# Optimization experiments

Measured on AMD Instinct MI355X. Metric: run time of the kernel, lower is better.

## Reference

```python
import jax, jax.numpy as jnp
import numpy as np

B, C, Hd, Wd = 8, 256, 64, 64
NUM_HEAD = 4
RATIO = 0.25
OUT_CH = int(NUM_HEAD * C * RATIO)      # 256
HEAD_DIM = OUT_CH // NUM_HEAD           # 64
EPS = 1e-5


def conv1x1(x, w, b=None):
    # x: [B,Ci,H,W], w: [Co,Ci]
    y = jnp.einsum('bchw,oc->bohw', x, w)
    if b is not None:
        y = y + b[None, :, None, None]
    return y


def setup_inputs() -> dict:
    key = jax.random.key(0)
    ks = jax.random.split(key, 16)
    s = lambda fan: 1.0 / np.sqrt(fan)
    return {
        'key':   jax.random.normal(ks[0], (B, C, Hd, Wd), jnp.float32),
        'query': jax.random.normal(ks[1], (B, C, Hd, Wd), jnp.float32),
        'wq': jax.random.normal(ks[2], (OUT_CH, C), jnp.float32) * s(C),
        'bq': jax.random.normal(ks[3], (OUT_CH,), jnp.float32) * 0.01,
        'wk': jax.random.normal(ks[4], (OUT_CH, C), jnp.float32) * s(C),
        'bk': jax.random.normal(ks[5], (OUT_CH,), jnp.float32) * 0.01,
        'wv': jax.random.normal(ks[6], (OUT_CH, C), jnp.float32) * s(C),
        'bv': jax.random.normal(ks[7], (OUT_CH,), jnp.float32) * 0.01,
        'wW': jax.random.normal(ks[8], (C, HEAD_DIM), jnp.float32) * s(HEAD_DIM),
        'bn_gamma': jnp.ones((C,), jnp.float32),
        'bn_beta': jnp.zeros((C,), jnp.float32),
        'bn_mean': jax.random.normal(ks[9], (C,), jnp.float32) * 0.1,
        'bn_var': jax.random.uniform(ks[10], (C,), jnp.float32, 0.5, 1.5),
        'w3': jax.random.normal(ks[11], (C, 2 * C, 3, 3), jnp.float32) * s(2 * C * 9),
        'b3': jax.random.normal(ks[12], (C,), jnp.float32) * 0.01,
        'w1': jax.random.normal(ks[13], (C, C), jnp.float32) * s(C),
        'b1': jax.random.normal(ks[14], (C,), jnp.float32) * 0.01,
    }


def reference(key, query, wq, bq, wk, bk, wv, bv, wW,
              bn_gamma, bn_beta, bn_mean, bn_var, w3, b3, w1, b1):
    b, c, h, w = query.shape
    q = conv1x1(query, wq, bq).reshape(b, NUM_HEAD, HEAD_DIM, h, w)
    k = conv1x1(key, wk, bk).reshape(b, NUM_HEAD, HEAD_DIM, h, w)
    v = conv1x1(key, wv, bv).reshape(b, NUM_HEAD, HEAD_DIM, h, w)

    att = (q * k).sum(axis=2) / np.sqrt(OUT_CH)          # [b, num_head, h, w]
    sm = jax.nn.softmax(att, axis=1)[:, :, None]         # softmax over heads
    weighted = (v * sm).sum(axis=1)                      # [b, head_dim, h, w]

    # W: 1x1 conv (no bias) + BatchNorm (inference)
    out = conv1x1(weighted, wW)
    inv = bn_gamma / jnp.sqrt(bn_var + EPS)
    out = out * inv[None, :, None, None] + (bn_beta - bn_mean * inv)[None, :, None, None]

    # fuse: ConvBlock (reflect-pad 3x3 conv + ELU) then 1x1 conv
    x = jnp.concatenate([key, out], axis=1)              # [b, 2C, h, w]
    x = jnp.pad(x, ((0, 0), (0, 0), (1, 1), (1, 1)), mode='reflect')
    x = jax.lax.conv_general_dilated(x, w3, (1, 1), 'VALID',
                                     dimension_numbers=('NCHW', 'OIHW', 'NCHW'))
    x = jax.nn.elu(x + b3[None, :, None, None])
    return conv1x1(x, w1, b1)
```

## Files before the change

kernel.cpp:

```cpp
#include <hip/hip_runtime.h>
#include <hip/hip_bf16.h>

typedef unsigned short u16;
typedef unsigned int u32;
typedef short bf16x8 __attribute__((ext_vector_type(8)));
typedef float f32x4 __attribute__((ext_vector_type(4)));

#define NPX 32768

__device__ __forceinline__ u16 f2bf(float f) {
  union { float f; u32 u; } v; v.f = f;
  return (u16)((v.u + 0x7FFFu + ((v.u >> 16) & 1u)) >> 16);
}

__device__ __forceinline__ void gload16(const u16* g, u16* l) {
  __builtin_amdgcn_global_load_lds(
      (const __attribute__((address_space(1))) void*)g,
      (__attribute__((address_space(3))) void*)l, 16, 0, 0);
}


__global__ __launch_bounds__(256) void prep_small(
    const float* __restrict__ wq, const float* __restrict__ wk,
    const float* __restrict__ wv, const float* __restrict__ w1,
    const float* __restrict__ wW, const float* __restrict__ gamma,
    const float* __restrict__ beta, const float* __restrict__ mean,
    const float* __restrict__ var,
    u16* __restrict__ wqb, u16* __restrict__ wkb, u16* __restrict__ wvb,
    u16* __restrict__ w1b, u16* __restrict__ wWpb, float* __restrict__ bWp) {
  int idx = blockIdx.x * 256 + threadIdx.x;
  if (idx < 65536) {
    int o = idx >> 8, c = idx & 255;
    int dst = (c >> 5) * 8192 + o * 32 + ((c >> 3) & 3) * 8 + (c & 7);
    wqb[dst] = f2bf(wq[idx]);
    wkb[dst] = f2bf(wk[idx]);
    wvb[dst] = f2bf(wv[idx]);
    w1b[dst] = f2bf(w1[idx]);
  } else if (idx < 65536 + 16384) {
    int j = idx - 65536;
    int o = j >> 6, c = j & 63;
    float inv = gamma[o] * rsqrtf(var[o] + 1e-5f);
    int dst = (c >> 5) * 8192 + o * 32 + ((c >> 3) & 3) * 8 + (c & 7);
    wWpb[dst] = f2bf(wW[j] * inv);
  } else if (idx < 65536 + 16384 + 256) {
    int o = idx - 65536 - 16384;
    float inv = gamma[o] * rsqrtf(var[o] + 1e-5f);
    bWp[o] = beta[o] - mean[o] * inv;
  }
}

__global__ __launch_bounds__(256) void prep_w3t(const float* __restrict__ w3,
                                                u16* __restrict__ w3c) {
  int idx = blockIdx.x * 256 + threadIdx.x;
  int o = idx >> 9, c = idx & 511;
  int cb = c >> 5;
  int lk = (c >> 3) & 3, e = c & 7;
  #pragma unroll
  for (int t = 0; t < 9; ++t)
    w3c[(size_t)(cb * 9 + t) * 8192 + o * 32 + lk * 8 + e] =
        f2bf(w3[idx * 9 + t]);
}

__global__ __launch_bounds__(256, 2) void attn_kernel(
    const float* __restrict__ qsrc, const float* __restrict__ ksrc,
    u16* __restrict__ xcat,
    const u16* __restrict__ wqb, const u16* __restrict__ wkb, const u16* __restrict__ wvb,
    const float* __restrict__ bq, const float* __restrict__ bk, const float* __restrict__ bv,
    const u16* __restrict__ wWpb, const float* __restrict__ bWp) {
  __shared__ __align__(16) char smem[74752];
  u16* aq = (u16*)smem;
  u16* ak = (u16*)(smem + 32768);
  u16* tile = (u16*)(smem + 65536);
  float* att_s = (float*)(smem + 65536);
  u16* wsum = (u16*)(smem + 66560);
  float* wbuf = (float*)smem;
  u16* ob = (u16*)smem;

  int tid = threadIdx.x;
  int lane = tid & 63, wv_ = tid >> 6;
  int lc = lane & 15, lk = lane >> 4;
  int px0 = blockIdx.x * 64;
  int b = px0 >> 12, hw0 = px0 & 4095;

  #pragma unroll
  for (int t = 0; t < 8; ++t) {
    const float* src = (t < 4) ? qsrc : ksrc;
    int cc = t & 3;
    #pragma unroll
    for (int i = 0; i < 4; ++i) {
      int idx = tid + 256 * i;
      int c = idx >> 4, p4 = idx & 15;
      const float4 v = *(const float4*)&src[(size_t)(b * 256 + cc * 64 + c) * 4096 + hw0 + p4 * 4];
      u32 lo = f2bf(v.x) | ((u32)f2bf(v.y) << 16);
      u32 hi = f2bf(v.z) | ((u32)f2bf(v.w) << 16);
      *(uint2*)&tile[c * 72 + p4 * 4] = make_uint2(lo, hi);
    }
    __syncthreads();
    int px = tid >> 2, cq = tid & 3;
    u32 vv[8];
    #pragma unroll
    for (int i = 0; i < 8; ++i) {
      u16 a = tile[(cq * 16 + 2 * i) * 72 + px];
      u16 bb = tile[(cq * 16 + 2 * i + 1) * 72 + px];
      vv[i] = a | ((u32)bb << 16);
    }
    u16* dstl = (t < 4) ? aq : ak;
    int c8 = cc * 8 + cq * 2;
    *(uint4*)(dstl + px * 256 + (c8 ^ (px & 7)) * 8) = make_uint4(vv[0], vv[1], vv[2], vv[3]);
    *(uint4*)(dstl + px * 256 + ((c8 + 1) ^ (px & 7)) * 8) = make_uint4(vv[4], vv[5], vv[6], vv[7]);
    if (t >= 4) {
      u16* dp = xcat + (size_t)(px0 + px) * 512 + cc * 64 + cq * 16;
      *(uint4*)dp = make_uint4(vv[0], vv[1], vv[2], vv[3]);
      *(uint4*)(dp + 8) = make_uint4(vv[4], vv[5], vv[6], vv[7]);
    }
    __syncthreads();
  }

  f32x4 zero4 = {0.f, 0.f, 0.f, 0.f};
  f32x4 accq[4][4], acck[4][4];
  #pragma unroll
  for (int mi = 0; mi < 4; ++mi)
    #pragma unroll
    for (int nj = 0; nj < 4; ++nj) { accq[mi][nj] = zero4; acck[mi][nj] = zero4; }

  #pragma unroll
  for (int kk = 0; kk < 8; ++kk) {
    bf16x8 afq[4], afk[4], bfq[4], bfk[4];
    #pragma unroll
    for (int mi = 0; mi < 4; ++mi) {
      int px = mi * 16 + lc;
      int s = (kk * 4 + lk) ^ (px & 7);
      afq[mi] = *(const bf16x8*)(aq + px * 256 + s * 8);
      afk[mi] = *(const bf16x8*)(ak + px * 256 + s * 8);
    }
    #pragma unroll
    for (int nj = 0; nj < 4; ++nj) {
      int n = wv_ * 64 + nj * 16 + lc;
      bfq[nj] = *(const bf16x8*)(wqb + kk * 8192 + n * 32 + lk * 8);
      bfk[nj] = *(const bf16x8*)(wkb + kk * 8192 + n * 32 + lk * 8);
    }
    #pragma unroll
    for (int mi = 0; mi < 4; ++mi)
      #pragma unroll
      for (int nj = 0; nj < 4; ++nj) {
        accq[mi][nj] = __builtin_amdgcn_mfma_f32_16x16x32_bf16(afq[mi], bfq[nj], accq[mi][nj], 0, 0, 0);
        acck[mi][nj] = __builtin_amdgcn_mfma_f32_16x16x32_bf16(afk[mi], bfk[nj], acck[mi][nj], 0, 0, 0);
      }
  }

  #pragma unroll
  for (int nj = 0; nj < 4; ++nj) {
    float bqv = bq[wv_ * 64 + nj * 16 + lc];
    float bkv = bk[wv_ * 64 + nj * 16 + lc];
    #pragma unroll
    for (int mi = 0; mi < 4; ++mi)
      #pragma unroll
      for (int j = 0; j < 4; ++j) { accq[mi][nj][j] += bqv; acck[mi][nj][j] += bkv; }
  }

  float smx[4][4];
  #pragma unroll
  for (int mi = 0; mi < 4; ++mi)
    #pragma unroll
    for (int j = 0; j < 4; ++j) {
      float p = 0.f;
      #pragma unroll
      for (int nj = 0; nj < 4; ++nj) p += accq[mi][nj][j] * acck[mi][nj][j];
      p += __shfl_xor(p, 1);
      p += __shfl_xor(p, 2);
      p += __shfl_xor(p, 4);
      p += __shfl_xor(p, 8);
      float a = p * 0.0625f;
      smx[mi][j] = a;
      if (lc == 0) att_s[wv_ * 64 + mi * 16 + lk * 4 + j] = a;
    }
  __syncthreads();
  #pragma unroll
  for (int mi = 0; mi < 4; ++mi)
    #pragma unroll
    for (int j = 0; j < 4; ++j) {
      int px = mi * 16 + lk * 4 + j;
      float a0 = att_s[px], a1 = att_s[64 + px], a2 = att_s[128 + px], a3 = att_s[192 + px];
      float mx = fmaxf(fmaxf(a0, a1), fmaxf(a2, a3));
      float e0 = __expf(a0 - mx), e1 = __expf(a1 - mx);
      float e2 = __expf(a2 - mx), e3 = __expf(a3 - mx);
      float den = e0 + e1 + e2 + e3;
      float ew = wv_ == 0 ? e0 : (wv_ == 1 ? e1 : (wv_ == 2 ? e2 : e3));
      smx[mi][j] = ew / den;
    }

  f32x4 accv[4][4];
  #pragma unroll
  for (int mi = 0; mi < 4; ++mi)
    #pragma unroll
    for (int nj = 0; nj < 4; ++nj) accv[mi][nj] = zero4;
  #pragma unroll
  for (int kk = 0; kk < 8; ++kk) {
    bf16x8 af[4], bfr[4];
    #pragma unroll
    for (int mi = 0; mi < 4; ++mi) {
      int px = mi * 16 + lc;
      int s = (kk * 4 + lk) ^ (px & 7);
      af[mi] = *(const bf16x8*)(ak + px * 256 + s * 8);
    }
    #pragma unroll
    for (int nj = 0; nj < 4; ++nj) {
      int n = wv_ * 64 + nj * 16 + lc;
      bfr[nj] = *(const bf16x8*)(wvb + kk * 8192 + n * 32 + lk * 8);
    }
    #pragma unroll
    for (int mi = 0; mi < 4; ++mi)
      #pragma unroll
      for (int nj = 0; nj < 4; ++nj)
        accv[mi][nj] = __builtin_amdgcn_mfma_f32_16x16x32_bf16(af[mi], bfr[nj], accv[mi][nj], 0, 0, 0);
  }
  #pragma unroll
  for (int nj = 0; nj < 4; ++nj) {
    float bvv = bv[wv_ * 64 + nj * 16 + lc];
    #pragma unroll
    for (int mi = 0; mi < 4; ++mi)
      #pragma unroll
      for (int j = 0; j < 4; ++j) accv[mi][nj][j] += bvv;
  }
  __syncthreads();

  #pragma unroll
  for (int mi = 0; mi < 4; ++mi)
    #pragma unroll
    for (int nj = 0; nj < 4; ++nj)
      #pragma unroll
      for (int j = 0; j < 4; ++j) {
        int px = mi * 16 + lk * 4 + j;
        wbuf[(wv_ * 64 + px) * 64 + nj * 16 + lc] = smx[mi][j] * accv[mi][nj][j];
      }
  __syncthreads();

  #pragma unroll
  for (int i = 0; i < 2; ++i) {
    int idx = tid + 256 * i;
    int px = idx >> 3, c = idx & 7;
    float a8[8] = {0.f, 0.f, 0.f, 0.f, 0.f, 0.f, 0.f, 0.f};
    #pragma unroll
    for (int h = 0; h < 4; ++h) {
      const float4* p = (const float4*)(wbuf + ((h * 64 + px) * 64 + c * 8));
      float4 u0 = p[0], u1 = p[1];
      a8[0] += u0.x; a8[1] += u0.y; a8[2] += u0.z; a8[3] += u0.w;
      a8[4] += u1.x; a8[5] += u1.y; a8[6] += u1.z; a8[7] += u1.w;
    }
    u32 p0 = f2bf(a8[0]) | ((u32)f2bf(a8[1]) << 16);
    u32 p1 = f2bf(a8[2]) | ((u32)f2bf(a8[3]) << 16);
    u32 p2 = f2bf(a8[4]) | ((u32)f2bf(a8[5]) << 16);
    u32 p3 = f2bf(a8[6]) | ((u32)f2bf(a8[7]) << 16);
    *(uint4*)(wsum + px * 64 + (c ^ (px & 7)) * 8) = make_uint4(p0, p1, p2, p3);
  }
  __syncthreads();

  f32x4 a4[4][4];
  #pragma unroll
  for (int mi = 0; mi < 4; ++mi)
    #pragma unroll
    for (int nj = 0; nj < 4; ++nj) a4[mi][nj] = zero4;
  #pragma unroll
  for (int kk = 0; kk < 2; ++kk) {
    bf16x8 af[4], bfr[4];
    #pragma unroll
    for (int mi = 0; mi < 4; ++mi) {
      int px = mi * 16 + lc;
      int s = (kk * 4 + lk) ^ (px & 7);
      af[mi] = *(const bf16x8*)(wsum + px * 64 + s * 8);
    }
    #pragma unroll
    for (int nj = 0; nj < 4; ++nj) {
      int n = wv_ * 64 + nj * 16 + lc;
      bfr[nj] = *(const bf16x8*)(wWpb + kk * 8192 + n * 32 + lk * 8);
    }
    #pragma unroll
    for (int mi = 0; mi < 4; ++mi)
      #pragma unroll
      for (int nj = 0; nj < 4; ++nj)
        a4[mi][nj] = __builtin_amdgcn_mfma_f32_16x16x32_bf16(af[mi], bfr[nj], a4[mi][nj], 0, 0, 0);
  }
  #pragma unroll
  for (int nj = 0; nj < 4; ++nj) {
    int o = wv_ * 64 + nj * 16 + lc;
    float bb = bWp[o];
    #pragma unroll
    for (int mi = 0; mi < 4; ++mi)
      #pragma unroll
      for (int j = 0; j < 4; ++j) {
        int px = mi * 16 + lk * 4 + j;
        ob[px * 264 + o] = f2bf(a4[mi][nj][j] + bb);
      }
  }
  __syncthreads();
  #pragma unroll
  for (int i = 0; i < 8; ++i) {
    int idx = tid + 256 * i;
    int px = idx >> 5, c8 = idx & 31;
    *(uint4*)(xcat + (size_t)(px0 + px) * 512 + 256 + c8 * 8) =
        *(const uint4*)(ob + px * 264 + c8 * 8);
  }
}

__global__ __launch_bounds__(512, 2) void conv3_kernel(
    const u16* __restrict__ xcat, const u16* __restrict__ w3c,
    const float* __restrict__ b3, const u16* __restrict__ w1b,
    const float* __restrict__ b1, float* __restrict__ out) {
  extern __shared__ __align__(16) u16 smem[];
  u16* xb0 = smem;
  u16* xb1 = smem + 8704;
  u16* wbase = smem + 17408;

  int tid = threadIdx.x;
  int lane = tid & 63, wave = tid >> 6;
  int lc = lane & 15, lk = lane >> 4;
  int wr = wave >> 2, wc = wave & 3;
  int sbid = (blockIdx.x & 7) * 32 + (blockIdx.x >> 3);
  int b = sbid >> 5, r0 = (sbid & 31) * 2;

  int gx0, gx1, gx2;
  #pragma unroll
  for (int i = 0; i < 3; ++i) {
    int c = (i == 0) ? tid : (i == 1 ? tid + 512 : 1024 + lane);
    int row = c / 272, rem = c - row * 272;
    int s = rem / 68, px = rem - s * 68;
    px = px < 66 ? px : 65;
    int h_in = r0 - 1 + row; h_in = h_in < 0 ? 1 : (h_in > 63 ? 62 : h_in);
    int w_in = px - 1;       w_in = w_in < 0 ? 1 : (w_in > 63 ? 62 : w_in);
    int g = ((b * 64 + h_in) * 64 + w_in) * 512 + s * 8;
    if (i == 0) gx0 = g; else if (i == 1) gx1 = g; else gx2 = g;
  }
  int gw0 = (tid ^ ((tid >> 3) & 7)) * 8;
  int p1_ = tid + 512;
  int gw1 = (p1_ ^ ((p1_ >> 3) & 7)) * 8;

#define STAGE_W(dst, slab)                                                      \
  do {                                                                          \
    const u16* ws_ = w3c + (size_t)(slab) * 8192;                               \
    gload16(ws_ + gw0, (dst) + (size_t)tid * 8);                                \
    gload16(ws_ + gw1, (dst) + (size_t)(tid + 512) * 8);                        \
  } while (0)

#define STAGE_X(dst, cb_)                                                       \
  do {                                                                          \
    gload16(xcat + gx0 + (cb_) * 32, (dst) + (size_t)tid * 8);                  \
    gload16(xcat + gx1 + (cb_) * 32, (dst) + (size_t)(tid + 512) * 8);          \
    if (wave == 0) gload16(xcat + gx2 + (cb_) * 32, (dst) + (size_t)(1024 + lane) * 8); \
  } while (0)

  f32x4 zero4 = {0.f, 0.f, 0.f, 0.f};
  f32x4 acc[4][4];
  #pragma unroll
  for (int mi = 0; mi < 4; ++mi)
    #pragma unroll
    for (int nj = 0; nj < 4; ++nj) acc[mi][nj] = zero4;

#define COMPUTE(TAP, XB, WIDX)                                                  \
  do {                                                                          \
    const u16* wcur_ = wbase + (size_t)(WIDX) * 8192;                           \
    bf16x8 af[4], bfr[4];                                                       \
    _Pragma("unroll") for (int mi = 0; mi < 4; ++mi)                            \
      af[mi] = *(const bf16x8*)((XB) +                                          \
          (size_t)(((wr + (TAP) / 3) * 4 + lk) * 68 + mi * 16 + lc + (TAP) % 3) * 8); \
    _Pragma("unroll") for (int nj = 0; nj < 4; ++nj) {                          \
      int j_ = (wc * 64 + nj * 16 + lc) * 4 + lk;                               \
      bfr[nj] = *(const bf16x8*)(wcur_ + (size_t)(j_ ^ ((j_ >> 3) & 7)) * 8);   \
    }                                                                           \
    __builtin_amdgcn_s_setprio(1);                                              \
    _Pragma("unroll") for (int mi = 0; mi < 4; ++mi)                            \
      _Pragma("unroll") for (int nj = 0; nj < 4; ++nj)                          \
        acc[mi][nj] = __builtin_amdgcn_mfma_f32_16x16x32_bf16(                  \
            af[mi], bfr[nj], acc[mi][nj], 0, 0, 0);                             \
    __builtin_amdgcn_s_setprio(0);                                              \
  } while (0)

  STAGE_W(wbase, 0);
  STAGE_W(wbase + 8192, 1);
  STAGE_X(xb0, 0);
  asm volatile("s_waitcnt vmcnt(0)\n\ts_barrier" ::: "memory");

  for (int cb = 0; cb < 15; ++cb) {
    const u16* xcur = (cb & 1) ? xb1 : xb0;
    u16* xnxt = (cb & 1) ? xb0 : xb1;
    int c4 = cb & 3;
    int base = cb * 9;
#define PH(TAP)                                                                 \
    STAGE_W(wbase + (size_t)((c4 + (TAP) + 2) & 3) * 8192, base + (TAP) + 2);   \
    if ((TAP) == 4) STAGE_X(xnxt, cb + 1);                                      \
    if ((TAP) < 4) {                                                            \
      asm volatile("s_waitcnt vmcnt(4)\n\ts_barrier" ::: "memory");             \
    } else if (wave == 0) {                                                     \
      asm volatile("s_waitcnt vmcnt(7)\n\ts_barrier" ::: "memory");             \
    } else {                                                                    \
      asm volatile("s_waitcnt vmcnt(6)\n\ts_barrier" ::: "memory");             \
    }                                                                           \
    COMPUTE(TAP, xcur, (c4 + (TAP)) & 3);
    PH(0) PH(1) PH(2) PH(3) PH(4) PH(5) PH(6) PH(7) PH(8)
#undef PH
  }
  {
    const u16* xcur = xb1;
#define PH15(TAP, WN)                                                           \
    if ((TAP) < 7) STAGE_W(wbase + (size_t)((3 + (TAP) + 2) & 3) * 8192, 137 + (TAP)); \
    asm volatile("s_waitcnt vmcnt(" #WN ")\n\ts_barrier" ::: "memory");         \
    COMPUTE(TAP, xcur, (3 + (TAP)) & 3);
    PH15(0, 4) PH15(1, 4) PH15(2, 4) PH15(3, 4) PH15(4, 4) PH15(5, 4) PH15(6, 4)
    PH15(7, 2) PH15(8, 0)
#undef PH15
  }
#undef STAGE_W
#undef STAGE_X
#undef COMPUTE

  __syncthreads();

  u16* eb = smem;
  #pragma unroll
  for (int nj = 0; nj < 4; ++nj) {
    int o = wc * 64 + nj * 16 + lc;
    float bias = b3[o];
    #pragma unroll
    for (int mi = 0; mi < 4; ++mi)
      #pragma unroll
      for (int j = 0; j < 4; ++j) {
        int p = wr * 64 + mi * 16 + lk * 4 + j;
        float v = acc[mi][nj][j] + bias;
        v = v > 0.f ? v : (__expf(v) - 1.f);
        eb[p * 260 + o] = f2bf(v);
      }
  }
  __syncthreads();

  f32x4 acc2[4][4];
  #pragma unroll
  for (int mi = 0; mi < 4; ++mi)
    #pragma unroll
    for (int nj = 0; nj < 4; ++nj) acc2[mi][nj] = zero4;
  #pragma unroll
  for (int kk = 0; kk < 8; ++kk) {
    bf16x8 af[4], bfr[4];
    #pragma unroll
    for (int mi = 0; mi < 4; ++mi)
      af[mi] = *(const bf16x8*)(eb + (size_t)(wr * 64 + mi * 16 + lc) * 260 + kk * 32 + lk * 8);
    #pragma unroll
    for (int nj = 0; nj < 4; ++nj)
      bfr[nj] = *(const bf16x8*)(w1b + kk * 8192 + (wc * 64 + nj * 16 + lc) * 32 + lk * 8);
    #pragma unroll
    for (int mi = 0; mi < 4; ++mi)
      #pragma unroll
      for (int nj = 0; nj < 4; ++nj)
        acc2[mi][nj] = __builtin_amdgcn_mfma_f32_16x16x32_bf16(af[mi], bfr[nj], acc2[mi][nj], 0, 0, 0);
  }
  #pragma unroll
  for (int nj = 0; nj < 4; ++nj) {
    int o = wc * 64 + nj * 16 + lc;
    float bias = b1[o];
    #pragma unroll
    for (int mi = 0; mi < 4; ++mi) {
      float4 v;
      v.x = acc2[mi][nj][0] + bias;
      v.y = acc2[mi][nj][1] + bias;
      v.z = acc2[mi][nj][2] + bias;
      v.w = acc2[mi][nj][3] + bias;
      *(float4*)&out[(size_t)(b * 256 + o) * 4096 + (r0 + wr) * 64 + mi * 16 + lk * 4] = v;
    }
  }
}

extern "C" void kernel_launch(void* const* d_in, const int* in_sizes, int n_in,
                              void* d_out, int out_size, void* d_ws, size_t ws_size,
                              hipStream_t stream) {
  const float* key   = (const float*)d_in[0];
  const float* query = (const float*)d_in[1];
  const float* wq    = (const float*)d_in[2];
  const float* bq    = (const float*)d_in[3];
  const float* wk    = (const float*)d_in[4];
  const float* bk    = (const float*)d_in[5];
  const float* wv    = (const float*)d_in[6];
  const float* bv    = (const float*)d_in[7];
  const float* wW    = (const float*)d_in[8];
  const float* gamma = (const float*)d_in[9];
  const float* beta  = (const float*)d_in[10];
  const float* mean  = (const float*)d_in[11];
  const float* var   = (const float*)d_in[12];
  const float* w3    = (const float*)d_in[13];
  const float* b3    = (const float*)d_in[14];
  const float* w1    = (const float*)d_in[15];
  const float* b1    = (const float*)d_in[16];
  float* out = (float*)d_out;

  char* ws = (char*)d_ws;
  u16* xcat  = (u16*)(ws + 16777216);
  u16* w3t   = (u16*)(ws + 67108864);
  u16* wqb   = (u16*)(ws + 69468160);
  u16* wkb   = (u16*)(ws + 69599232);
  u16* wvb   = (u16*)(ws + 69730304);
  u16* w1b   = (u16*)(ws + 69861376);
  u16* wWpb  = (u16*)(ws + 69992448);
  float* bWp = (float*)(ws + 70025216);

  (void)hipFuncSetAttribute((const void*)conv3_kernel,
                            hipFuncAttributeMaxDynamicSharedMemorySize, 100352);

  prep_small<<<321, 256, 0, stream>>>(wq, wk, wv, w1, wW, gamma, beta, mean, var,
                                      wqb, wkb, wvb, w1b, wWpb, bWp);
  prep_w3t<<<512, 256, 0, stream>>>(w3, w3t);
  attn_kernel<<<512, 256, 0, stream>>>(query, key, xcat, wqb, wkb, wvb,
                                       bq, bk, bv, wWpb, bWp);
  conv3_kernel<<<256, 512, 100352, stream>>>(xcat, w3t, b3, w1b, b1, out);
}
```

Before: 122.6 us.

## Load conv3 weights straight into registers and drop LDS weight staging

The 3x3 conv kernel no longer stages weight slabs through shared memory. Each wave now reads its B-fragments from global memory into a three-deep register ring, prefetched three taps ahead. The activation tile layout changes to pixel-major with four channel slots, the per-tap barriers are removed so there is only one barrier per channel block, and shared memory shrinks to a static 66 KB array. This cuts LDS traffic and synchronisation, at the cost of more VGPRs, the loss of the 2-blocks-per-CU launch bound, and weight loads that each wave issues redundantly from global/L2.

```diff
diff --git a/kernel.cpp b/kernel.cpp
--- a/kernel.cpp
+++ b/kernel.cpp
@@ -302,14 +302,13 @@
   }
 }
 
-__global__ __launch_bounds__(512, 2) void conv3_kernel(
+__global__ __launch_bounds__(512) void conv3_kernel(
     const u16* __restrict__ xcat, const u16* __restrict__ w3c,
     const float* __restrict__ b3, const u16* __restrict__ w1b,
     const float* __restrict__ b1, float* __restrict__ out) {
-  extern __shared__ __align__(16) u16 smem[];
+  __shared__ __align__(16) u16 smem[33792];
   u16* xb0 = smem;
   u16* xb1 = smem + 8704;
-  u16* wbase = smem + 17408;
 
   int tid = threadIdx.x;
   int lane = tid & 63, wave = tid >> 6;
@@ -322,30 +321,32 @@
   #pragma unroll
   for (int i = 0; i < 3; ++i) {
     int c = (i == 0) ? tid : (i == 1 ? tid + 512 : 1024 + lane);
-    int row = c / 272, rem = c - row * 272;
-    int s = rem / 68, px = rem - s * 68;
+    int q = c >> 2, slot = c & 3;
+    int row = q / 68, px = q - row * 68;
     px = px < 66 ? px : 65;
     int h_in = r0 - 1 + row; h_in = h_in < 0 ? 1 : (h_in > 63 ? 62 : h_in);
     int w_in = px - 1;       w_in = w_in < 0 ? 1 : (w_in > 63 ? 62 : w_in);
-    int g = ((b * 64 + h_in) * 64 + w_in) * 512 + s * 8;
+    int g = ((b * 64 + h_in) * 64 + w_in) * 512 + slot * 8;
     if (i == 0) gx0 = g; else if (i == 1) gx1 = g; else gx2 = g;
   }
-  int gw0 = (tid ^ ((tid >> 3) & 7)) * 8;
-  int p1_ = tid + 512;
-  int gw1 = (p1_ ^ ((p1_ >> 3) & 7)) * 8;
-
-#define STAGE_W(dst, slab)                                                      \
-  do {                                                                          \
-    const u16* ws_ = w3c + (size_t)(slab) * 8192;                               \
-    gload16(ws_ + gw0, (dst) + (size_t)tid * 8);                                \
-    gload16(ws_ + gw1, (dst) + (size_t)(tid + 512) * 8);                        \
-  } while (0)
+  int wo0 = ((wc * 64 + lc) * 4 + lk) * 8;
 
 #define STAGE_X(dst, cb_)                                                       \
   do {                                                                          \
+    asm volatile("" ::: "memory");                                              \
     gload16(xcat + gx0 + (cb_) * 32, (dst) + (size_t)tid * 8);                  \
     gload16(xcat + gx1 + (cb_) * 32, (dst) + (size_t)(tid + 512) * 8);          \
-    if (wave == 0) gload16(xcat + gx2 + (cb_) * 32, (dst) + (size_t)(1024 + lane) * 8); \
+    gload16(xcat + gx2 + (cb_) * 32, (dst) + (size_t)(1024 + lane) * 8);        \
+    asm volatile("" ::: "memory");                                              \
+  } while (0)
+
+#define PREF_W(SLOT, SLAB)                                                      \
+  do {                                                                          \
+    const u16* ws_ = w3c + (size_t)(SLAB) * 8192 + wo0;                         \
+    Wr[SLOT][0] = *(const bf16x8*)(ws_);                                        \
+    Wr[SLOT][1] = *(const bf16x8*)(ws_ + 512);                                  \
+    Wr[SLOT][2] = *(const bf16x8*)(ws_ + 1024);                                 \
+    Wr[SLOT][3] = *(const bf16x8*)(ws_ + 1536);                                 \
   } while (0)
 
   f32x4 zero4 = {0.f, 0.f, 0.f, 0.f};
@@ -355,62 +356,41 @@
     #pragma unroll
     for (int nj = 0; nj < 4; ++nj) acc[mi][nj] = zero4;
 
-#define COMPUTE(TAP, XB, WIDX)                                                  \
-  do {                                                                          \
-    const u16* wcur_ = wbase + (size_t)(WIDX) * 8192;                           \
-    bf16x8 af[4], bfr[4];                                                       \
-    _Pragma("unroll") for (int mi = 0; mi < 4; ++mi)                            \
-      af[mi] = *(const bf16x8*)((XB) +                                          \
-          (size_t)(((wr + (TAP) / 3) * 4 + lk) * 68 + mi * 16 + lc + (TAP) % 3) * 8); \
-    _Pragma("unroll") for (int nj = 0; nj < 4; ++nj) {                          \
-      int j_ = (wc * 64 + nj * 16 + lc) * 4 + lk;                               \
-      bfr[nj] = *(const bf16x8*)(wcur_ + (size_t)(j_ ^ ((j_ >> 3) & 7)) * 8);   \
-    }                                                                           \
-    __builtin_amdgcn_s_setprio(1);                                              \
-    _Pragma("unroll") for (int mi = 0; mi < 4; ++mi)                            \
-      _Pragma("unroll") for (int nj = 0; nj < 4; ++nj)                          \
-        acc[mi][nj] = __builtin_amdgcn_mfma_f32_16x16x32_bf16(                  \
-            af[mi], bfr[nj], acc[mi][nj], 0, 0, 0);                             \
-    __builtin_amdgcn_s_setprio(0);                                              \
-  } while (0)
-
-  STAGE_W(wbase, 0);
-  STAGE_W(wbase + 8192, 1);
+  bf16x8 Wr[3][4];
+
   STAGE_X(xb0, 0);
-  asm volatile("s_waitcnt vmcnt(0)\n\ts_barrier" ::: "memory");
-
-  for (int cb = 0; cb < 15; ++cb) {
+  PREF_W(0, 0);
+  PREF_W(1, 1);
+  PREF_W(2, 2);
+  asm volatile("s_waitcnt vmcnt(12)\n\ts_barrier" ::: "memory");
+
+  for (int cb = 0; cb < 16; ++cb) {
     const u16* xcur = (cb & 1) ? xb1 : xb0;
     u16* xnxt = (cb & 1) ? xb0 : xb1;
-    int c4 = cb & 3;
-    int base = cb * 9;
-#define PH(TAP)                                                                 \
-    STAGE_W(wbase + (size_t)((c4 + (TAP) + 2) & 3) * 8192, base + (TAP) + 2);   \
-    if ((TAP) == 4) STAGE_X(xnxt, cb + 1);                                      \
-    if ((TAP) < 4) {                                                            \
-      asm volatile("s_waitcnt vmcnt(4)\n\ts_barrier" ::: "memory");             \
-    } else if (wave == 0) {                                                     \
-      asm volatile("s_waitcnt vmcnt(7)\n\ts_barrier" ::: "memory");             \
-    } else {                                                                    \
-      asm volatile("s_waitcnt vmcnt(6)\n\ts_barrier" ::: "memory");             \
-    }                                                                           \
-    COMPUTE(TAP, xcur, (c4 + (TAP)) & 3);
-    PH(0) PH(1) PH(2) PH(3) PH(4) PH(5) PH(6) PH(7) PH(8)
-#undef PH
-  }
-  {
-    const u16* xcur = xb1;
-#define PH15(TAP, WN)                                                           \
-    if ((TAP) < 7) STAGE_W(wbase + (size_t)((3 + (TAP) + 2) & 3) * 8192, 137 + (TAP)); \
-    asm volatile("s_waitcnt vmcnt(" #WN ")\n\ts_barrier" ::: "memory");         \
-    COMPUTE(TAP, xcur, (3 + (TAP)) & 3);
-    PH15(0, 4) PH15(1, 4) PH15(2, 4) PH15(3, 4) PH15(4, 4) PH15(5, 4) PH15(6, 4)
-    PH15(7, 2) PH15(8, 0)
-#undef PH15
-  }
-#undef STAGE_W
+#define TAP(T)                                                                  \
+    {                                                                           \
+      const int dy = (T) / 3, dx = (T) % 3;                                     \
+      bf16x8 af[4];                                                             \
+      _Pragma("unroll") for (int mi = 0; mi < 4; ++mi)                          \
+        af[mi] = *(const bf16x8*)(xcur +                                        \
+            (size_t)(((wr + dy) * 68 + mi * 16 + lc + dx) * 4 + lk) * 8);       \
+      __builtin_amdgcn_s_setprio(1);                                            \
+      _Pragma("unroll") for (int mi = 0; mi < 4; ++mi)                          \
+        _Pragma("unroll") for (int nj = 0; nj < 4; ++nj)                        \
+          acc[mi][nj] = __builtin_amdgcn_mfma_f32_16x16x32_bf16(                \
+              af[mi], Wr[(T) % 3][nj], acc[mi][nj], 0, 0, 0);                   \
+      __builtin_amdgcn_s_setprio(0);                                            \
+      int slab_ = cb * 9 + (T) + 3;                                             \
+      if (slab_ < 144) PREF_W((T) % 3, slab_);                                  \
+      if ((T) == 5 && cb < 15) STAGE_X(xnxt, cb + 1);                           \
+    }
+    TAP(0) TAP(1) TAP(2) TAP(3) TAP(4) TAP(5) TAP(6) TAP(7) TAP(8)
+#undef TAP
+    if (cb < 15)
+      asm volatile("s_waitcnt vmcnt(12)\n\ts_barrier" ::: "memory");
+  }
 #undef STAGE_X
-#undef COMPUTE
+#undef PREF_W
 
   __syncthreads();
 
@@ -426,7 +406,7 @@
         int p = wr * 64 + mi * 16 + lk * 4 + j;
         float v = acc[mi][nj][j] + bias;
         v = v > 0.f ? v : (__expf(v) - 1.f);
-        eb[p * 260 + o] = f2bf(v);
+        eb[p * 264 + o] = f2bf(v);
       }
   }
   __syncthreads();
@@ -441,7 +421,7 @@
     bf16x8 af[4], bfr[4];
     #pragma unroll
     for (int mi = 0; mi < 4; ++mi)
-      af[mi] = *(const bf16x8*)(eb + (size_t)(wr * 64 + mi * 16 + lc) * 260 + kk * 32 + lk * 8);
+      af[mi] = *(const bf16x8*)(eb + (size_t)(wr * 64 + mi * 16 + lc) * 264 + kk * 32 + lk * 8);
     #pragma unroll
     for (int nj = 0; nj < 4; ++nj)
       bfr[nj] = *(const bf16x8*)(w1b + kk * 8192 + (wc * 64 + nj * 16 + lc) * 32 + lk * 8);
@@ -499,13 +479,10 @@
   u16* wWpb  = (u16*)(ws + 69992448);
   float* bWp = (float*)(ws + 70025216);
 
-  (void)hipFuncSetAttribute((const void*)conv3_kernel,
-                            hipFuncAttributeMaxDynamicSharedMemorySize, 100352);
-
   prep_small<<<321, 256, 0, stream>>>(wq, wk, wv, w1, wW, gamma, beta, mean, var,
                                       wqb, wkb, wvb, w1b, wWpb, bWp);
   prep_w3t<<<512, 256, 0, stream>>>(w3, w3t);
   attn_kernel<<<512, 256, 0, stream>>>(query, key, xcat, wqb, wkb, wvb,
                                        bq, bk, bv, wWpb, bWp);
-  conv3_kernel<<<256, 512, 100352, stream>>>(xcat, w3t, b3, w1b, b1, out);
-}
+  conv3_kernel<<<256, 512, 0, stream>>>(xcat, w3t, b3, w1b, b1, out);
+}
```

Result: slower. 128.5 us (+4.8%).

## Restructure conv3 pipeline: 3-slot weight ring, swizzled X tile, reordered barriers

Applied to the files above, without the earlier changes.

The conv3 main loop now uses a 3-slot weight ring instead of 4 slots, and stores the input halo tile in an XOR-swizzled packed layout meant to avoid LDS bank conflicts. LDS fragments are read before the next global-to-LDS loads are issued, with barriers on both sides of the MFMA block, so loads overlap compute with fewer waits. It also drops the occupancy hint in launch_bounds, changes the epilogue pitch and trims shared memory to 96KB. The extra barriers per tap and the lost min-blocks hint could reduce overlap or occupancy.

```diff
diff --git a/kernel.cpp b/kernel.cpp
--- a/kernel.cpp
+++ b/kernel.cpp
@@ -18,7 +18,6 @@
       (const __attribute__((address_space(1))) void*)g,
       (__attribute__((address_space(3))) void*)l, 16, 0, 0);
 }
-
 
 __global__ __launch_bounds__(256) void prep_small(
     const float* __restrict__ wq, const float* __restrict__ wk,
@@ -302,14 +301,14 @@
   }
 }
 
-__global__ __launch_bounds__(512, 2) void conv3_kernel(
+__global__ __launch_bounds__(512) void conv3_kernel(
     const u16* __restrict__ xcat, const u16* __restrict__ w3c,
     const float* __restrict__ b3, const u16* __restrict__ w1b,
     const float* __restrict__ b1, float* __restrict__ out) {
   extern __shared__ __align__(16) u16 smem[];
   u16* xb0 = smem;
-  u16* xb1 = smem + 8704;
-  u16* wbase = smem + 17408;
+  u16* xb1 = smem + 12288;
+  u16* wring = smem + 24576;
 
   int tid = threadIdx.x;
   int lane = tid & 63, wave = tid >> 6;
@@ -321,31 +320,34 @@
   int gx0, gx1, gx2;
   #pragma unroll
   for (int i = 0; i < 3; ++i) {
-    int c = (i == 0) ? tid : (i == 1 ? tid + 512 : 1024 + lane);
-    int row = c / 272, rem = c - row * 272;
-    int s = rem / 68, px = rem - s * 68;
-    px = px < 66 ? px : 65;
+    int pc = tid + 512 * i;
+    int pcm = pc < 1056 ? pc : pc - 1056;
+    int G = pcm >> 3;
+    int el = (pcm & 7) ^ (G & 7);
+    int row = G / 33, q2 = G - row * 33;
+    int px = q2 * 2 + (el >> 2), slot = el & 3;
     int h_in = r0 - 1 + row; h_in = h_in < 0 ? 1 : (h_in > 63 ? 62 : h_in);
     int w_in = px - 1;       w_in = w_in < 0 ? 1 : (w_in > 63 ? 62 : w_in);
-    int g = ((b * 64 + h_in) * 64 + w_in) * 512 + s * 8;
+    int g = ((b * 64 + h_in) * 64 + w_in) * 512 + slot * 8;
     if (i == 0) gx0 = g; else if (i == 1) gx1 = g; else gx2 = g;
   }
   int gw0 = (tid ^ ((tid >> 3) & 7)) * 8;
-  int p1_ = tid + 512;
-  int gw1 = (p1_ ^ ((p1_ >> 3) & 7)) * 8;
-
-#define STAGE_W(dst, slab)                                                      \
-  do {                                                                          \
-    const u16* ws_ = w3c + (size_t)(slab) * 8192;                               \
-    gload16(ws_ + gw0, (dst) + (size_t)tid * 8);                                \
-    gload16(ws_ + gw1, (dst) + (size_t)(tid + 512) * 8);                        \
-  } while (0)
+  int pw1 = tid + 512;
+  int gw1 = (pw1 ^ ((pw1 >> 3) & 7)) * 8;
 
 #define STAGE_X(dst, cb_)                                                       \
   do {                                                                          \
     gload16(xcat + gx0 + (cb_) * 32, (dst) + (size_t)tid * 8);                  \
     gload16(xcat + gx1 + (cb_) * 32, (dst) + (size_t)(tid + 512) * 8);          \
-    if (wave == 0) gload16(xcat + gx2 + (cb_) * 32, (dst) + (size_t)(1024 + lane) * 8); \
+    gload16(xcat + gx2 + (cb_) * 32, (dst) + (size_t)(tid + 1024) * 8);         \
+  } while (0)
+
+#define STAGE_W(slot_, slab_)                                                   \
+  do {                                                                          \
+    const u16* ws_ = w3c + (size_t)(slab_) * 8192;                              \
+    u16* wd_ = wring + (size_t)(slot_) * 8192;                                  \
+    gload16(ws_ + gw0, wd_ + (size_t)tid * 8);                                  \
+    gload16(ws_ + gw1, wd_ + (size_t)(tid + 512) * 8);                          \
   } while (0)
 
   f32x4 zero4 = {0.f, 0.f, 0.f, 0.f};
@@ -355,64 +357,61 @@
     #pragma unroll
     for (int nj = 0; nj < 4; ++nj) acc[mi][nj] = zero4;
 
-#define COMPUTE(TAP, XB, WIDX)                                                  \
-  do {                                                                          \
-    const u16* wcur_ = wbase + (size_t)(WIDX) * 8192;                           \
+#define PH(TAP, DO_W, DO_X, WN)                                                 \
+  {                                                                             \
+    const int dy = (TAP) / 3, dx = (TAP) % 3;                                   \
     bf16x8 af[4], bfr[4];                                                       \
-    _Pragma("unroll") for (int mi = 0; mi < 4; ++mi)                            \
-      af[mi] = *(const bf16x8*)((XB) +                                          \
-          (size_t)(((wr + (TAP) / 3) * 4 + lk) * 68 + mi * 16 + lc + (TAP) % 3) * 8); \
+    _Pragma("unroll") for (int mi = 0; mi < 4; ++mi) {                          \
+      int px = mi * 16 + lc + dx;                                               \
+      int G = (wr + dy) * 33 + (px >> 1);                                       \
+      int el = (px & 1) * 4 + lk;                                               \
+      af[mi] = *(const bf16x8*)(xcur + (size_t)(G * 8 + (el ^ (G & 7))) * 8);   \
+    }                                                                           \
     _Pragma("unroll") for (int nj = 0; nj < 4; ++nj) {                          \
-      int j_ = (wc * 64 + nj * 16 + lc) * 4 + lk;                               \
-      bfr[nj] = *(const bf16x8*)(wcur_ + (size_t)(j_ ^ ((j_ >> 3) & 7)) * 8);   \
+      int j = (wc * 64 + nj * 16 + lc) * 4 + lk;                                \
+      bfr[nj] = *(const bf16x8*)(wring + (size_t)((TAP) % 3) * 8192 +           \
+                                 (size_t)(j ^ ((j >> 3) & 7)) * 8);             \
     }                                                                           \
+    if (DO_W) STAGE_W(((TAP) + 2) % 3, cb * 9 + (TAP) + 2);                     \
+    if (DO_X) STAGE_X(xnxt, cb + 1);                                            \
+    __builtin_amdgcn_s_barrier();                                               \
+    asm volatile("s_waitcnt lgkmcnt(0)" ::: "memory");                          \
+    __builtin_amdgcn_sched_barrier(0);                                          \
     __builtin_amdgcn_s_setprio(1);                                              \
     _Pragma("unroll") for (int mi = 0; mi < 4; ++mi)                            \
       _Pragma("unroll") for (int nj = 0; nj < 4; ++nj)                          \
         acc[mi][nj] = __builtin_amdgcn_mfma_f32_16x16x32_bf16(                  \
             af[mi], bfr[nj], acc[mi][nj], 0, 0, 0);                             \
     __builtin_amdgcn_s_setprio(0);                                              \
-  } while (0)
-
-  STAGE_W(wbase, 0);
-  STAGE_W(wbase + 8192, 1);
+    asm volatile("s_waitcnt vmcnt(" WN ")" ::: "memory");                       \
+    __builtin_amdgcn_s_barrier();                                               \
+  }
+
+  STAGE_W(0, 0);
+  STAGE_W(1, 1);
   STAGE_X(xb0, 0);
-  asm volatile("s_waitcnt vmcnt(0)\n\ts_barrier" ::: "memory");
+  asm volatile("s_waitcnt vmcnt(0)" ::: "memory");
+  __builtin_amdgcn_s_barrier();
 
   for (int cb = 0; cb < 15; ++cb) {
     const u16* xcur = (cb & 1) ? xb1 : xb0;
     u16* xnxt = (cb & 1) ? xb0 : xb1;
-    int c4 = cb & 3;
-    int base = cb * 9;
-#define PH(TAP)                                                                 \
-    STAGE_W(wbase + (size_t)((c4 + (TAP) + 2) & 3) * 8192, base + (TAP) + 2);   \
-    if ((TAP) == 4) STAGE_X(xnxt, cb + 1);                                      \
-    if ((TAP) < 4) {                                                            \
-      asm volatile("s_waitcnt vmcnt(4)\n\ts_barrier" ::: "memory");             \
-    } else if (wave == 0) {                                                     \
-      asm volatile("s_waitcnt vmcnt(7)\n\ts_barrier" ::: "memory");             \
-    } else {                                                                    \
-      asm volatile("s_waitcnt vmcnt(6)\n\ts_barrier" ::: "memory");             \
-    }                                                                           \
-    COMPUTE(TAP, xcur, (c4 + (TAP)) & 3);
-    PH(0) PH(1) PH(2) PH(3) PH(4) PH(5) PH(6) PH(7) PH(8)
+    PH(0, 1, 0, "2") PH(1, 1, 0, "2") PH(2, 1, 0, "2") PH(3, 1, 0, "2")
+    PH(4, 1, 1, "5") PH(5, 1, 0, "5")
+    PH(6, 1, 0, "2") PH(7, 1, 0, "2") PH(8, 1, 0, "2")
+  }
+  {
+    const int cb = 15;
+    const u16* xcur = xb1;
+    u16* xnxt = xb0;
+    (void)xnxt;
+    PH(0, 1, 0, "2") PH(1, 1, 0, "2") PH(2, 1, 0, "2") PH(3, 1, 0, "2")
+    PH(4, 1, 0, "2") PH(5, 1, 0, "2") PH(6, 1, 0, "2")
+    PH(7, 0, 0, "0") PH(8, 0, 0, "0")
+  }
 #undef PH
-  }
-  {
-    const u16* xcur = xb1;
-#define PH15(TAP, WN)                                                           \
-    if ((TAP) < 7) STAGE_W(wbase + (size_t)((3 + (TAP) + 2) & 3) * 8192, 137 + (TAP)); \
-    asm volatile("s_waitcnt vmcnt(" #WN ")\n\ts_barrier" ::: "memory");         \
-    COMPUTE(TAP, xcur, (3 + (TAP)) & 3);
-    PH15(0, 4) PH15(1, 4) PH15(2, 4) PH15(3, 4) PH15(4, 4) PH15(5, 4) PH15(6, 4)
-    PH15(7, 2) PH15(8, 0)
-#undef PH15
-  }
+#undef STAGE_X
 #undef STAGE_W
-#undef STAGE_X
-#undef COMPUTE
-
-  __syncthreads();
 
   u16* eb = smem;
   #pragma unroll
@@ -426,7 +425,7 @@
         int p = wr * 64 + mi * 16 + lk * 4 + j;
         float v = acc[mi][nj][j] + bias;
         v = v > 0.f ? v : (__expf(v) - 1.f);
-        eb[p * 260 + o] = f2bf(v);
+        eb[p * 264 + o] = f2bf(v);
       }
   }
   __syncthreads();
@@ -441,7 +440,7 @@
     bf16x8 af[4], bfr[4];
     #pragma unroll
     for (int mi = 0; mi < 4; ++mi)
-      af[mi] = *(const bf16x8*)(eb + (size_t)(wr * 64 + mi * 16 + lc) * 260 + kk * 32 + lk * 8);
+      af[mi] = *(const bf16x8*)(eb + (size_t)(wr * 64 + mi * 16 + lc) * 264 + kk * 32 + lk * 8);
     #pragma unroll
     for (int nj = 0; nj < 4; ++nj)
       bfr[nj] = *(const bf16x8*)(w1b + kk * 8192 + (wc * 64 + nj * 16 + lc) * 32 + lk * 8);
@@ -500,12 +499,12 @@
   float* bWp = (float*)(ws + 70025216);
 
   (void)hipFuncSetAttribute((const void*)conv3_kernel,
-                            hipFuncAttributeMaxDynamicSharedMemorySize, 100352);
+                            hipFuncAttributeMaxDynamicSharedMemorySize, 98304);
 
   prep_small<<<321, 256, 0, stream>>>(wq, wk, wv, w1, wW, gamma, beta, mean, var,
                                       wqb, wkb, wvb, w1b, wWpb, bWp);
   prep_w3t<<<512, 256, 0, stream>>>(w3, w3t);
   attn_kernel<<<512, 256, 0, stream>>>(query, key, xcat, wqb, wkb, wvb,
                                        bq, bk, bv, wWpb, bWp);
-  conv3_kernel<<<256, 512, 100352, stream>>>(xcat, w3t, b3, w1b, b1, out);
-}
+  conv3_kernel<<<256, 512, 98304, stream>>>(xcat, w3t, b3, w1b, b1, out);
+}
```

New measurement: 117.9 us. 3.9% less time.
